# Performance work log

Hardware: AMD Instinct MI355X
Metric: run time of the kernel (lower is better)

## Reference

```python
import jax, jax.numpy as jnp
import numpy as np

EMBED = 1024
HEADS = 16
HEAD_DIM = EMBED // HEADS


def setup_inputs() -> dict:
    key = jax.random.key(0)
    ks = jax.random.split(key, 8)
    N, L = 4, 2048
    values = jax.random.normal(ks[0], (N, L, EMBED), dtype=jnp.float32)
    keys_ = jax.random.normal(ks[1], (N, L, EMBED), dtype=jnp.float32)
    queries = jax.random.normal(ks[2], (N, L, EMBED), dtype=jnp.float32)
    s = 1.0 / np.sqrt(HEAD_DIM)
    Wv = jax.random.normal(ks[3], (HEAD_DIM, HEAD_DIM), dtype=jnp.float32) * s
    Wk = jax.random.normal(ks[4], (HEAD_DIM, HEAD_DIM), dtype=jnp.float32) * s
    Wq = jax.random.normal(ks[5], (HEAD_DIM, HEAD_DIM), dtype=jnp.float32) * s
    Wo = jax.random.normal(ks[6], (EMBED, EMBED), dtype=jnp.float32) * (1.0 / np.sqrt(EMBED))
    bo = jnp.zeros((EMBED,), dtype=jnp.float32)
    return {"values": values, "keys": keys_, "queries": queries,
            "Wv": Wv, "Wk": Wk, "Wq": Wq, "Wo": Wo, "bo": bo}


def reference(values, keys, queries, Wv, Wk, Wq, Wo, bo):
    N, L, _ = queries.shape
    # split heads: [N, L, H, D]
    v = values.reshape(N, -1, HEADS, HEAD_DIM)
    k = keys.reshape(N, -1, HEADS, HEAD_DIM)
    q = queries.reshape(N, L, HEADS, HEAD_DIM)
    # per-head linear (same [D,D] weight shared across heads), torch Linear: x @ W.T
    v = jnp.einsum('nlhd,ed->nlhe', v, Wv)
    k = jnp.einsum('nlhd,ed->nlhe', k, Wk)
    q = jnp.einsum('nqhd,ed->nqhe', q, Wq)
    # attention scores [N, H, Q, K], scaled by sqrt(embed_size) as in source
    scores = jnp.einsum('nqhd,nkhd->nhqk', q, k) / jnp.sqrt(jnp.float32(EMBED))
    attn = jax.nn.softmax(scores, axis=-1)
    out = jnp.einsum('nhqk,nkhd->nqhd', attn, v).reshape(N, L, EMBED)
    return out @ Wo.T + bo
```

## Files before the change

kernel.cpp:

```cpp
#include <hip/hip_runtime.h>
#include <math.h>

#define EMBED 1024
#define HEADS 16
#define HD    64
#define NB    4
#define LSEQ  2048

typedef __attribute__((ext_vector_type(8))) short bf16x8;
typedef __attribute__((ext_vector_type(16))) float f32x16;

typedef __attribute__((address_space(1))) void as1_void;
typedef __attribute__((address_space(3))) void as3_void;

__device__ __forceinline__ void gload_lds16(const void* g, void* l) {
    __builtin_amdgcn_global_load_lds((const as1_void*)g, (as3_void*)l, 16, 0, 0);
}

__device__ inline bf16x8 as_bf16x8(uint4 u) {
    union { uint4 u; bf16x8 b; } c; c.u = u; return c.b;
}
__device__ inline unsigned short bf16r(float x) {
    unsigned u = __float_as_uint(x);
    u += 0x7fffu + ((u >> 16) & 1u);
    return (unsigned short)(u >> 16);
}
__device__ inline float bfh2f(unsigned short h) {
    return __uint_as_float(((unsigned)h) << 16);
}
__device__ inline void split2(float x, float y, unsigned& hw, unsigned& lw) {
    unsigned short hx = bf16r(x), hy = bf16r(y);
    unsigned short lx = bf16r(x - bfh2f(hx)), ly = bf16r(y - bfh2f(hy));
    hw = (unsigned)hx | ((unsigned)hy << 16);
    lw = (unsigned)lx | ((unsigned)ly << 16);
}

__global__ __launch_bounds__(256, 3) void proj_kernel(
    const float* __restrict__ Xv, const float* __restrict__ Xk, const float* __restrict__ Xq,
    const float* __restrict__ Wv, const float* __restrict__ Wk, const float* __restrict__ Wq,
    unsigned short* __restrict__ Vt, unsigned short* __restrict__ Kp, unsigned short* __restrict__ Qp)
{
    __shared__ uint4 sXh[128 * 8];
    __shared__ uint4 sXl[128 * 8];
    __shared__ uint4 sWh[64 * 8];
    __shared__ uint4 sWl[64 * 8];

    const int t = threadIdx.x;
    const int lane = t & 63, w = t >> 6;
    const int l5 = lane & 31, hi = lane >> 5;
    const int h  = blockIdx.y;
    const int n  = blockIdx.x >> 4;
    const int l0 = (blockIdx.x & 15) * 128;

    const float QSC = 1.44269504088896341f / 32.0f;
    const float* Xs[3] = {Xv, Xk, Xq};
    const float* Ws[3] = {Wv, Wk, Wq};

    const int frow = t >> 4;
    const int fcol = t & 15;

    for (int p = 0; p < 3; ++p) {
        __syncthreads();
        {
            const float* xb = Xs[p] + ((size_t)(n * LSEQ + l0 + frow)) * EMBED + h * HD + fcol * 4;
            unsigned short* dh = (unsigned short*)sXh;
            unsigned short* dl = (unsigned short*)sXl;
            #pragma unroll
            for (int i = 0; i < 8; ++i) {
                int row = frow + i * 16;
                float4 v = *(const float4*)(xb + (size_t)i * 16 * EMBED);
                int gg = fcol >> 1, s8 = (fcol & 1) * 4;
                int idx = row * 64 + ((gg ^ (row & 7)) * 8) + s8;
                uint2 hv, lv;
                split2(v.x, v.y, hv.x, lv.x);
                split2(v.z, v.w, hv.y, lv.y);
                *(uint2*)(dh + idx) = hv;
                *(uint2*)(dl + idx) = lv;
            }
        }
        #pragma unroll
        for (int i = 0; i < 2; ++i) {
            int u = t + 256 * i;
            int e = u >> 3, g = u & 7;
            const float* wb = Ws[p] + u * 8;
            float4 v0 = *(const float4*)(wb);
            float4 v1 = *(const float4*)(wb + 4);
            uint4 hq, lq;
            split2(v0.x, v0.y, hq.x, lq.x);
            split2(v0.z, v0.w, hq.y, lq.y);
            split2(v1.x, v1.y, hq.z, lq.z);
            split2(v1.z, v1.w, hq.w, lq.w);
            int idx = e * 8 + (g ^ (e & 7));
            sWh[idx] = hq;
            sWl[idx] = lq;
        }
        __syncthreads();

        f32x16 acc0, acc1;
        #pragma unroll
        for (int i = 0; i < 16; ++i) { acc0[i] = 0.f; acc1[i] = 0.f; }

        const int xrow = w * 32 + l5;
        const int w0r = l5, w1r = 32 + l5;
        #pragma unroll
        for (int kc = 0; kc < 4; ++kc) {
            int gsel = kc * 2 + hi;
            bf16x8 xh = as_bf16x8(sXh[xrow * 8 + (gsel ^ (xrow & 7))]);
            bf16x8 xl = as_bf16x8(sXl[xrow * 8 + (gsel ^ (xrow & 7))]);
            bf16x8 wh0 = as_bf16x8(sWh[w0r * 8 + (gsel ^ (w0r & 7))]);
            bf16x8 wl0 = as_bf16x8(sWl[w0r * 8 + (gsel ^ (w0r & 7))]);
            bf16x8 wh1 = as_bf16x8(sWh[w1r * 8 + (gsel ^ (w1r & 7))]);
            bf16x8 wl1 = as_bf16x8(sWl[w1r * 8 + (gsel ^ (w1r & 7))]);
            if (p == 0) {
                acc0 = __builtin_amdgcn_mfma_f32_32x32x16_bf16(wh0, xh, acc0, 0, 0, 0);
                acc0 = __builtin_amdgcn_mfma_f32_32x32x16_bf16(wh0, xl, acc0, 0, 0, 0);
                acc0 = __builtin_amdgcn_mfma_f32_32x32x16_bf16(wl0, xh, acc0, 0, 0, 0);
                acc1 = __builtin_amdgcn_mfma_f32_32x32x16_bf16(wh1, xh, acc1, 0, 0, 0);
                acc1 = __builtin_amdgcn_mfma_f32_32x32x16_bf16(wh1, xl, acc1, 0, 0, 0);
                acc1 = __builtin_amdgcn_mfma_f32_32x32x16_bf16(wl1, xh, acc1, 0, 0, 0);
            } else {
                acc0 = __builtin_amdgcn_mfma_f32_32x32x16_bf16(xh, wh0, acc0, 0, 0, 0);
                acc0 = __builtin_amdgcn_mfma_f32_32x32x16_bf16(xh, wl0, acc0, 0, 0, 0);
                acc0 = __builtin_amdgcn_mfma_f32_32x32x16_bf16(xl, wh0, acc0, 0, 0, 0);
                acc1 = __builtin_amdgcn_mfma_f32_32x32x16_bf16(xh, wh1, acc1, 0, 0, 0);
                acc1 = __builtin_amdgcn_mfma_f32_32x32x16_bf16(xh, wl1, acc1, 0, 0, 0);
                acc1 = __builtin_amdgcn_mfma_f32_32x32x16_bf16(xl, wh1, acc1, 0, 0, 0);
            }
        }

        if (p == 0) {
            unsigned short* vb = Vt + (((size_t)(n * HEADS + h)) * HD) * LSEQ + l0 + w * 32 + l5;
            #pragma unroll
            for (int r = 0; r < 16; ++r) {
                int er = (r & 3) + 8 * (r >> 2) + 4 * hi;
                vb[(size_t)er * LSEQ]        = bf16r(acc0[r]);
                vb[(size_t)(32 + er) * LSEQ] = bf16r(acc1[r]);
            }
        } else {
            unsigned short* dst = (p == 1) ? Kp : Qp;
            float sc = (p == 2) ? QSC : 1.0f;
            unsigned short* db = dst + (((size_t)(n * HEADS + h)) * LSEQ + l0 + w * 32) * HD;
            #pragma unroll
            for (int r = 0; r < 16; ++r) {
                int tok = (r & 3) + 8 * (r >> 2) + 4 * hi;
                db[(size_t)tok * HD + l5]      = bf16r(acc0[r] * sc);
                db[(size_t)tok * HD + 32 + l5] = bf16r(acc1[r] * sc);
            }
        }
    }
}

__global__ __launch_bounds__(256, 4) void attn_kernel(
    const unsigned short* __restrict__ Qp, const unsigned short* __restrict__ Kp,
    const unsigned short* __restrict__ Vt,
    unsigned short* __restrict__ AOh, unsigned short* __restrict__ AOl)
{
    __shared__ uint4 sK[128 * 8];
    __shared__ uint4 sV[64 * 16];

    const int t = threadIdx.x;
    const int lane = t & 63, w = t >> 6;
    const int l5 = lane & 31, hi = lane >> 5;
    const int n = blockIdx.z, h = blockIdx.y;
    const int q0 = blockIdx.x * 128;
    const size_t hoff = ((size_t)n * HEADS + h) * (size_t)(LSEQ * HD);
    const unsigned short* Kh = Kp + hoff;
    const unsigned short* Vh = Vt + hoff;

    bf16x8 qf[4];
    {
        const uint4* qg = (const uint4*)(Qp + hoff + (size_t)(q0 + w * 32 + l5) * HD);
        #pragma unroll
        for (int kc = 0; kc < 4; ++kc) qf[kc] = as_bf16x8(qg[kc * 2 + hi]);
    }

    f32x16 Oa0, Oa1;
    #pragma unroll
    for (int i = 0; i < 16; ++i) { Oa0[i] = 0.f; Oa1[i] = 0.f; }
    float lsum = 0.f;

    for (int kt = 0; kt < LSEQ; kt += 128) {
        const uint4* gK = (const uint4*)(Kh + (size_t)kt * HD);
        #pragma unroll
        for (int i = 0; i < 4; ++i) {
            int u = t + 256 * i; int key = u >> 3, gd = u & 7;
            sK[key * 8 + (gd ^ (key & 7))] = gK[u];
        }
        #pragma unroll
        for (int i = 0; i < 4; ++i) {
            int u = t + 256 * i; int d = u >> 4, kg = u & 15;
            sV[d * 16 + (kg ^ (d & 7))] = *(const uint4*)(Vh + (size_t)d * LSEQ + kt + kg * 8);
        }
        __syncthreads();

        #pragma unroll
        for (int tc = 0; tc < 4; ++tc) {
            f32x16 c;
            #pragma unroll
            for (int i = 0; i < 16; ++i) c[i] = 0.f;
            int key = tc * 32 + l5;
            #pragma unroll
            for (int kc = 0; kc < 4; ++kc) {
                bf16x8 kf = as_bf16x8(sK[key * 8 + ((kc * 2 + hi) ^ (l5 & 7))]);
                c = __builtin_amdgcn_mfma_f32_32x32x16_bf16(kf, qf[kc], c, 0, 0, 0);
            }

            unsigned pw[8];
            #pragma unroll
            for (int g = 0; g < 4; ++g) {
                float p0 = exp2f(c[4 * g]);
                float p1 = exp2f(c[4 * g + 1]);
                float p2 = exp2f(c[4 * g + 2]);
                float p3 = exp2f(c[4 * g + 3]);
                lsum += (p0 + p1) + (p2 + p3);
                asm("v_cvt_pk_bf16_f32 %0, %1, %2" : "=v"(pw[2 * g])     : "v"(p0), "v"(p1));
                asm("v_cvt_pk_bf16_f32 %0, %1, %2" : "=v"(pw[2 * g + 1]) : "v"(p2), "v"(p3));
            }
            asm("v_permlane32_swap_b32 %0, %1" : "+v"(pw[0]), "+v"(pw[2]));
            asm("v_permlane32_swap_b32 %0, %1" : "+v"(pw[1]), "+v"(pw[3]));
            asm("v_permlane32_swap_b32 %0, %1" : "+v"(pw[4]), "+v"(pw[6]));
            asm("v_permlane32_swap_b32 %0, %1" : "+v"(pw[5]), "+v"(pw[7]));

            #pragma unroll
            for (int win = 0; win < 2; ++win) {
                union { unsigned u[4]; bf16x8 b; } pf;
                pf.u[0] = pw[4 * win];
                pf.u[1] = pw[4 * win + 1];
                pf.u[2] = pw[4 * win + 2];
                pf.u[3] = pw[4 * win + 3];
                int vg = tc * 4 + (win << 1) + hi;
                bf16x8 v0 = as_bf16x8(sV[ l5       * 16 + (vg ^ (l5 & 7))]);
                Oa0 = __builtin_amdgcn_mfma_f32_32x32x16_bf16(pf.b, v0, Oa0, 0, 0, 0);
                bf16x8 v1 = as_bf16x8(sV[(32 + l5) * 16 + (vg ^ (l5 & 7))]);
                Oa1 = __builtin_amdgcn_mfma_f32_32x32x16_bf16(pf.b, v1, Oa1, 0, 0, 0);
            }
        }
        __syncthreads();
    }

    lsum += __shfl_xor(lsum, 32);
    float inv = 1.0f / lsum;
    float* sLf = (float*)sK;
    if (hi == 0) sLf[w * 32 + l5] = inv;

    unsigned short* hB = AOh + hoff;
    unsigned short* lB = AOl + hoff;
    #pragma unroll
    for (int r = 0; r < 16; ++r) {
        int qr = (r & 3) + 8 * (r >> 2) + 4 * hi;
        float invq = sLf[w * 32 + qr];
        size_t row = (size_t)(q0 + w * 32 + qr) * HD;
        float o0 = Oa0[r] * invq;
        float o1 = Oa1[r] * invq;
        unsigned short h0 = bf16r(o0), h1 = bf16r(o1);
        hB[row +      l5] = h0;
        hB[row + 32 + l5] = h1;
        lB[row +      l5] = bf16r(o0 - bfh2f(h0));
        lB[row + 32 + l5] = bf16r(o1 - bfh2f(h1));
    }
}

__global__ __launch_bounds__(256) void wsplit_kernel(
    const float* __restrict__ Wo,
    unsigned short* __restrict__ Woh, unsigned short* __restrict__ Wol)
{
    int i = blockIdx.x * 256 + threadIdx.x;
    float4 v = ((const float4*)Wo)[i];
    ushort4 h, l;
    h.x = bf16r(v.x); l.x = bf16r(v.x - bfh2f(h.x));
    h.y = bf16r(v.y); l.y = bf16r(v.y - bfh2f(h.y));
    h.z = bf16r(v.z); l.z = bf16r(v.z - bfh2f(h.z));
    h.w = bf16r(v.w); l.w = bf16r(v.w - bfh2f(h.w));
    ((ushort4*)Woh)[i] = h;
    ((ushort4*)Wol)[i] = l;
}

__global__ __launch_bounds__(256, 2) void outproj_kernel(
    const unsigned short* __restrict__ AOh, const unsigned short* __restrict__ AOl,
    const unsigned short* __restrict__ Woh, const unsigned short* __restrict__ Wol,
    const float* __restrict__ bo, float* __restrict__ out)
{
    __shared__ uint4 sAh[1024];
    __shared__ uint4 sAl[1024];
    __shared__ uint4 sBh[1024];
    __shared__ uint4 sBl[1024];

    const int t = threadIdx.x;
    const int lane = t & 63, w = t >> 6;
    const int l5 = lane & 31, hi = lane >> 5;
    const int m0 = blockIdx.x * 128;
    const int e0 = blockIdx.y * 128;
    const int n  = m0 >> 11, l0 = m0 & 2047;
    const int mr = (w & 1) * 64, nc = (w >> 1) * 64;

    f32x16 acc[2][2];
    #pragma unroll
    for (int a = 0; a < 2; ++a)
        #pragma unroll
        for (int b = 0; b < 2; ++b)
            #pragma unroll
            for (int i = 0; i < 16; ++i) acc[a][b][i] = 0.f;

    for (int hh = 0; hh < 16; ++hh) {
        const unsigned short* Ah = AOh + ((((size_t)n * HEADS + hh) * LSEQ) + l0) * HD;
        const unsigned short* Al = AOl + ((((size_t)n * HEADS + hh) * LSEQ) + l0) * HD;
        #pragma unroll
        for (int i = 0; i < 4; ++i) {
            int g = t + i * 256;
            gload_lds16(Ah + g * 8, sAh + g);
            gload_lds16(Al + g * 8, sAl + g);
            int e = g >> 3, gf = g & 7;
            size_t boff = (size_t)(e0 + e) * EMBED + hh * 64 + gf * 8;
            gload_lds16(Woh + boff, sBh + g);
            gload_lds16(Wol + boff, sBl + g);
        }
        __syncthreads();

        #pragma unroll
        for (int s = 0; s < 4; ++s) {
            int gcol = s * 2 + hi;
            bf16x8 ah0 = as_bf16x8(sAh[(mr +      l5) * 8 + gcol]);
            bf16x8 ah1 = as_bf16x8(sAh[(mr + 32 + l5) * 8 + gcol]);
            bf16x8 al0 = as_bf16x8(sAl[(mr +      l5) * 8 + gcol]);
            bf16x8 al1 = as_bf16x8(sAl[(mr + 32 + l5) * 8 + gcol]);
            bf16x8 bh0 = as_bf16x8(sBh[(nc +      l5) * 8 + gcol]);
            bf16x8 bh1 = as_bf16x8(sBh[(nc + 32 + l5) * 8 + gcol]);
            bf16x8 bl0 = as_bf16x8(sBl[(nc +      l5) * 8 + gcol]);
            bf16x8 bl1 = as_bf16x8(sBl[(nc + 32 + l5) * 8 + gcol]);

            acc[0][0] = __builtin_amdgcn_mfma_f32_32x32x16_bf16(ah0, bh0, acc[0][0], 0, 0, 0);
            acc[0][1] = __builtin_amdgcn_mfma_f32_32x32x16_bf16(ah0, bh1, acc[0][1], 0, 0, 0);
            acc[1][0] = __builtin_amdgcn_mfma_f32_32x32x16_bf16(ah1, bh0, acc[1][0], 0, 0, 0);
            acc[1][1] = __builtin_amdgcn_mfma_f32_32x32x16_bf16(ah1, bh1, acc[1][1], 0, 0, 0);

            acc[0][0] = __builtin_amdgcn_mfma_f32_32x32x16_bf16(ah0, bl0, acc[0][0], 0, 0, 0);
            acc[0][1] = __builtin_amdgcn_mfma_f32_32x32x16_bf16(ah0, bl1, acc[0][1], 0, 0, 0);
            acc[1][0] = __builtin_amdgcn_mfma_f32_32x32x16_bf16(ah1, bl0, acc[1][0], 0, 0, 0);
            acc[1][1] = __builtin_amdgcn_mfma_f32_32x32x16_bf16(ah1, bl1, acc[1][1], 0, 0, 0);

            acc[0][0] = __builtin_amdgcn_mfma_f32_32x32x16_bf16(al0, bh0, acc[0][0], 0, 0, 0);
            acc[0][1] = __builtin_amdgcn_mfma_f32_32x32x16_bf16(al0, bh1, acc[0][1], 0, 0, 0);
            acc[1][0] = __builtin_amdgcn_mfma_f32_32x32x16_bf16(al1, bh0, acc[1][0], 0, 0, 0);
            acc[1][1] = __builtin_amdgcn_mfma_f32_32x32x16_bf16(al1, bh1, acc[1][1], 0, 0, 0);
        }
        __syncthreads();
    }

    float b0 = bo[e0 + nc + l5];
    float b1 = bo[e0 + nc + 32 + l5];
    #pragma unroll
    for (int ti = 0; ti < 2; ++ti) {
        #pragma unroll
        for (int r = 0; r < 16; ++r) {
            int row = m0 + mr + ti * 32 + (r & 3) + 8 * (r >> 2) + 4 * hi;
            float* o = out + (size_t)row * EMBED + e0 + nc;
            o[l5]      = acc[ti][0][r] + b0;
            o[32 + l5] = acc[ti][1][r] + b1;
        }
    }
}

extern "C" void kernel_launch(void* const* d_in, const int* in_sizes, int n_in,
                              void* d_out, int out_size, void* d_ws, size_t ws_size,
                              hipStream_t stream)
{
    const float* values  = (const float*)d_in[0];
    const float* keys    = (const float*)d_in[1];
    const float* queries = (const float*)d_in[2];
    const float* Wv      = (const float*)d_in[3];
    const float* Wk      = (const float*)d_in[4];
    const float* Wq      = (const float*)d_in[5];
    const float* Wo      = (const float*)d_in[6];
    const float* bo      = (const float*)d_in[7];
    float* out = (float*)d_out;

    const size_t bufElems = (size_t)NB * HEADS * LSEQ * HD;
    unsigned short* Qp  = (unsigned short*)d_ws;
    unsigned short* Kp  = Qp  + bufElems;
    unsigned short* Vt  = Kp  + bufElems;
    unsigned short* AOh = Vt  + bufElems;
    unsigned short* AOl = AOh + bufElems;
    unsigned short* Woh = AOl + bufElems;
    unsigned short* Wol = Woh + (size_t)EMBED * EMBED;

    wsplit_kernel<<<dim3(1024), 256, 0, stream>>>(Wo, Woh, Wol);
    proj_kernel<<<dim3(NB * 16, HEADS), 256, 0, stream>>>(values, keys, queries, Wv, Wk, Wq, Vt, Kp, Qp);
    attn_kernel<<<dim3(LSEQ / 128, HEADS, NB), 256, 0, stream>>>(Qp, Kp, Vt, AOh, AOl);
    outproj_kernel<<<dim3(NB * LSEQ / 128, EMBED / 128), 256, 0, stream>>>(AOh, AOl, Woh, Wol, bo, out);
}
```

Baseline: 384.0 us.

## Prefetch next K/V tile into registers and raise wave priority around MFMAs

The attention loop now loads the next 128-key K and V tile from global memory into registers while the current tile is being computed, then stores those registers to LDS at the top of the next iteration. This hides global load latency behind the MFMA and softmax work. It also wraps the MFMA blocks in s_setprio to favour matrix issue, and splits the row-sum accumulator in two to shorten the add dependency chain. The register prefetch adds about 32 VGPRs per thread, which could reduce occupancy.

```diff
diff --git a/kernel.cpp b/kernel.cpp
--- a/kernel.cpp
+++ b/kernel.cpp
@@ -177,19 +177,38 @@
     f32x16 Oa0, Oa1;
     #pragma unroll
     for (int i = 0; i < 16; ++i) { Oa0[i] = 0.f; Oa1[i] = 0.f; }
-    float lsum = 0.f;
+    float ls0 = 0.f, ls1 = 0.f;
+
+    uint4 rK[4], rV[4];
+    {
+        const uint4* gK = (const uint4*)Kh;
+        #pragma unroll
+        for (int i = 0; i < 4; ++i) {
+            int u = t + 256 * i;
+            rK[i] = gK[u];
+            int d = u >> 4, kg = u & 15;
+            rV[i] = *(const uint4*)(Vh + (size_t)d * LSEQ + kg * 8);
+        }
+    }
 
     for (int kt = 0; kt < LSEQ; kt += 128) {
-        const uint4* gK = (const uint4*)(Kh + (size_t)kt * HD);
         #pragma unroll
         for (int i = 0; i < 4; ++i) {
-            int u = t + 256 * i; int key = u >> 3, gd = u & 7;
-            sK[key * 8 + (gd ^ (key & 7))] = gK[u];
-        }
-        #pragma unroll
-        for (int i = 0; i < 4; ++i) {
-            int u = t + 256 * i; int d = u >> 4, kg = u & 15;
-            sV[d * 16 + (kg ^ (d & 7))] = *(const uint4*)(Vh + (size_t)d * LSEQ + kt + kg * 8);
+            int u = t + 256 * i;
+            int key = u >> 3, gd = u & 7;
+            sK[key * 8 + (gd ^ (key & 7))] = rK[i];
+            int d = u >> 4, kg = u & 15;
+            sV[d * 16 + (kg ^ (d & 7))] = rV[i];
+        }
+        if (kt + 128 < LSEQ) {
+            const uint4* gK = (const uint4*)(Kh + (size_t)(kt + 128) * HD);
+            #pragma unroll
+            for (int i = 0; i < 4; ++i) {
+                int u = t + 256 * i;
+                rK[i] = gK[u];
+                int d = u >> 4, kg = u & 15;
+                rV[i] = *(const uint4*)(Vh + (size_t)d * LSEQ + (kt + 128) + kg * 8);
+            }
         }
         __syncthreads();
 
@@ -199,11 +218,13 @@
             #pragma unroll
             for (int i = 0; i < 16; ++i) c[i] = 0.f;
             int key = tc * 32 + l5;
+            __builtin_amdgcn_s_setprio(1);
             #pragma unroll
             for (int kc = 0; kc < 4; ++kc) {
                 bf16x8 kf = as_bf16x8(sK[key * 8 + ((kc * 2 + hi) ^ (l5 & 7))]);
                 c = __builtin_amdgcn_mfma_f32_32x32x16_bf16(kf, qf[kc], c, 0, 0, 0);
             }
+            __builtin_amdgcn_s_setprio(0);
 
             unsigned pw[8];
             #pragma unroll
@@ -212,7 +233,8 @@
                 float p1 = exp2f(c[4 * g + 1]);
                 float p2 = exp2f(c[4 * g + 2]);
                 float p3 = exp2f(c[4 * g + 3]);
-                lsum += (p0 + p1) + (p2 + p3);
+                ls0 += (p0 + p1);
+                ls1 += (p2 + p3);
                 asm("v_cvt_pk_bf16_f32 %0, %1, %2" : "=v"(pw[2 * g])     : "v"(p0), "v"(p1));
                 asm("v_cvt_pk_bf16_f32 %0, %1, %2" : "=v"(pw[2 * g + 1]) : "v"(p2), "v"(p3));
             }
@@ -221,6 +243,7 @@
             asm("v_permlane32_swap_b32 %0, %1" : "+v"(pw[4]), "+v"(pw[6]));
             asm("v_permlane32_swap_b32 %0, %1" : "+v"(pw[5]), "+v"(pw[7]));
 
+            __builtin_amdgcn_s_setprio(1);
             #pragma unroll
             for (int win = 0; win < 2; ++win) {
                 union { unsigned u[4]; bf16x8 b; } pf;
@@ -234,10 +257,12 @@
                 bf16x8 v1 = as_bf16x8(sV[(32 + l5) * 16 + (vg ^ (l5 & 7))]);
                 Oa1 = __builtin_amdgcn_mfma_f32_32x32x16_bf16(pf.b, v1, Oa1, 0, 0, 0);
             }
-        }
-        __syncthreads();
-    }
-
+            __builtin_amdgcn_s_setprio(0);
+        }
+        __syncthreads();
+    }
+
+    float lsum = ls0 + ls1;
     lsum += __shfl_xor(lsum, 32);
     float inv = 1.0f / lsum;
     float* sLf = (float*)sK;
```

New measurement: 498.8 us. 1.3x slower.

## Double-buffer K/V tiles with direct global-to-LDS loads in attention kernel

Applied to the files above, without the earlier changes.

The attention loop now uses 64-key tiles in two LDS buffers, filled with global_load_lds so the next tile's K/V load overlaps MFMA work on the current one. Explicit vmcnt waits and raw barriers replace the previous load-then-syncthreads pattern. The MFMA sections are wrapped in s_setprio, and the row-sum is split into two accumulators for more ILP. Smaller tiles mean twice as many barriers, and the hand-written waitcnt depends on each thread issuing exactly four loads per stage.

```diff
diff --git a/kernel.cpp b/kernel.cpp
--- a/kernel.cpp
+++ b/kernel.cpp
@@ -155,8 +155,8 @@
     const unsigned short* __restrict__ Vt,
     unsigned short* __restrict__ AOh, unsigned short* __restrict__ AOl)
 {
-    __shared__ uint4 sK[128 * 8];
-    __shared__ uint4 sV[64 * 16];
+    __shared__ uint4 sK[2][64 * 8];
+    __shared__ uint4 sV[2][64 * 8];
 
     const int t = threadIdx.x;
     const int lane = t & 63, w = t >> 6;
@@ -177,33 +177,48 @@
     f32x16 Oa0, Oa1;
     #pragma unroll
     for (int i = 0; i < 16; ++i) { Oa0[i] = 0.f; Oa1[i] = 0.f; }
-    float lsum = 0.f;
-
-    for (int kt = 0; kt < LSEQ; kt += 128) {
-        const uint4* gK = (const uint4*)(Kh + (size_t)kt * HD);
-        #pragma unroll
-        for (int i = 0; i < 4; ++i) {
-            int u = t + 256 * i; int key = u >> 3, gd = u & 7;
-            sK[key * 8 + (gd ^ (key & 7))] = gK[u];
-        }
-        #pragma unroll
-        for (int i = 0; i < 4; ++i) {
-            int u = t + 256 * i; int d = u >> 4, kg = u & 15;
-            sV[d * 16 + (kg ^ (d & 7))] = *(const uint4*)(Vh + (size_t)d * LSEQ + kt + kg * 8);
-        }
-        __syncthreads();
-
-        #pragma unroll
-        for (int tc = 0; tc < 4; ++tc) {
+    float ls0 = 0.f, ls1 = 0.f;
+
+    const int r0 = t >> 3;
+    const int g0 = (t & 7) ^ (r0 & 7);
+    const uint4* gK = (const uint4*)Kh;
+    const uint4* gV = (const uint4*)Vh;
+
+    #define STAGE(TILE, BUF)                                                        \
+        do {                                                                        \
+            int kb_ = (TILE) * 64;                                                  \
+            gload_lds16(gK + (size_t)(kb_ + r0) * 8 + g0,        &sK[BUF][t]);      \
+            gload_lds16(gK + (size_t)(kb_ + r0 + 32) * 8 + g0,   &sK[BUF][t + 256]);\
+            gload_lds16(gV + (size_t)r0 * 256 + (kb_ >> 3) + g0, &sV[BUF][t]);      \
+            gload_lds16(gV + (size_t)(r0 + 32) * 256 + (kb_ >> 3) + g0,             \
+                        &sV[BUF][t + 256]);                                         \
+        } while (0)
+
+    STAGE(0, 0);
+    int cur = 0;
+
+    for (int tt = 0; tt < LSEQ / 64; ++tt) {
+        if (tt + 1 < LSEQ / 64) {
+            STAGE(tt + 1, cur ^ 1);
+            asm volatile("s_waitcnt vmcnt(4)" ::: "memory");
+        } else {
+            asm volatile("s_waitcnt vmcnt(0)" ::: "memory");
+        }
+        __builtin_amdgcn_s_barrier();
+
+        #pragma unroll
+        for (int tc = 0; tc < 2; ++tc) {
             f32x16 c;
             #pragma unroll
             for (int i = 0; i < 16; ++i) c[i] = 0.f;
             int key = tc * 32 + l5;
+            __builtin_amdgcn_s_setprio(1);
             #pragma unroll
             for (int kc = 0; kc < 4; ++kc) {
-                bf16x8 kf = as_bf16x8(sK[key * 8 + ((kc * 2 + hi) ^ (l5 & 7))]);
+                bf16x8 kf = as_bf16x8(sK[cur][key * 8 + ((kc * 2 + hi) ^ (l5 & 7))]);
                 c = __builtin_amdgcn_mfma_f32_32x32x16_bf16(kf, qf[kc], c, 0, 0, 0);
             }
+            __builtin_amdgcn_s_setprio(0);
 
             unsigned pw[8];
             #pragma unroll
@@ -212,7 +227,8 @@
                 float p1 = exp2f(c[4 * g + 1]);
                 float p2 = exp2f(c[4 * g + 2]);
                 float p3 = exp2f(c[4 * g + 3]);
-                lsum += (p0 + p1) + (p2 + p3);
+                ls0 += (p0 + p1);
+                ls1 += (p2 + p3);
                 asm("v_cvt_pk_bf16_f32 %0, %1, %2" : "=v"(pw[2 * g])     : "v"(p0), "v"(p1));
                 asm("v_cvt_pk_bf16_f32 %0, %1, %2" : "=v"(pw[2 * g + 1]) : "v"(p2), "v"(p3));
             }
@@ -221,6 +237,7 @@
             asm("v_permlane32_swap_b32 %0, %1" : "+v"(pw[4]), "+v"(pw[6]));
             asm("v_permlane32_swap_b32 %0, %1" : "+v"(pw[5]), "+v"(pw[7]));
 
+            __builtin_amdgcn_s_setprio(1);
             #pragma unroll
             for (int win = 0; win < 2; ++win) {
                 union { unsigned u[4]; bf16x8 b; } pf;
@@ -229,19 +246,24 @@
                 pf.u[2] = pw[4 * win + 2];
                 pf.u[3] = pw[4 * win + 3];
                 int vg = tc * 4 + (win << 1) + hi;
-                bf16x8 v0 = as_bf16x8(sV[ l5       * 16 + (vg ^ (l5 & 7))]);
+                bf16x8 v0 = as_bf16x8(sV[cur][ l5       * 8 + (vg ^ (l5 & 7))]);
                 Oa0 = __builtin_amdgcn_mfma_f32_32x32x16_bf16(pf.b, v0, Oa0, 0, 0, 0);
-                bf16x8 v1 = as_bf16x8(sV[(32 + l5) * 16 + (vg ^ (l5 & 7))]);
+                bf16x8 v1 = as_bf16x8(sV[cur][(32 + l5) * 8 + (vg ^ (l5 & 7))]);
                 Oa1 = __builtin_amdgcn_mfma_f32_32x32x16_bf16(pf.b, v1, Oa1, 0, 0, 0);
             }
-        }
-        __syncthreads();
-    }
-
+            __builtin_amdgcn_s_setprio(0);
+        }
+        __builtin_amdgcn_s_barrier();
+        cur ^= 1;
+    }
+    #undef STAGE
+
+    float lsum = ls0 + ls1;
     lsum += __shfl_xor(lsum, 32);
     float inv = 1.0f / lsum;
-    float* sLf = (float*)sK;
+    float* sLf = (float*)&sK[0][0];
     if (hi == 0) sLf[w * 32 + l5] = inv;
+    __syncthreads();
 
     unsigned short* hB = AOh + hoff;
     unsigned short* lB = AOl + hoff;
```

Result: no change. 377.9 us (-1.6%).
